# Performance work log

Hardware: AMD Instinct MI355X
Metric: run time of the kernel (lower is better)

The kernel has to match this reference:

```python
import jax, jax.numpy as jnp
import numpy as np

COMMITMENT_COST = 0.25


def setup_inputs() -> dict:
    key = jax.random.key(0)
    k1, k2 = jax.random.split(key)
    inputs = jax.random.normal(k1, (32, 1024, 256), dtype=jnp.float32)
    codebook = jax.random.normal(k2, (8192, 256), dtype=jnp.float32)
    return {"inputs": inputs, "codebook": codebook}


def reference(inputs, codebook):
    input_shape = inputs.shape
    D = codebook.shape[1]
    K = codebook.shape[0]
    flat = inputs.reshape(-1, D)                      # [N, D]
    N = flat.shape[0]

    distances = (
        jnp.sum(flat * flat, axis=1, keepdims=True)
        + jnp.sum(codebook * codebook, axis=1)
        - 2.0 * flat @ codebook.T
    )                                                  # [N, K]
    idx = jnp.argmin(distances, axis=1)               # [N]

    # gather (equivalent to one-hot @ codebook)
    quantized = jnp.take(codebook, idx, axis=0).reshape(input_shape)

    # straight-through estimator
    quantized_st = inputs + jax.lax.stop_gradient(quantized - inputs)

    e_latent_loss = jnp.mean((jax.lax.stop_gradient(quantized_st) - inputs) ** 2)
    q_latent_loss = jnp.mean((quantized - jax.lax.stop_gradient(inputs)) ** 2)
    commitment_loss = COMMITMENT_COST * e_latent_loss
    codebook_loss = q_latent_loss
    vq_loss = commitment_loss + codebook_loss

    # perplexity of codebook usage (avg one-hot probs)
    counts = jnp.zeros((K,), dtype=inputs.dtype).at[idx].add(1.0)
    avg_probs = counts / N
    perplexity = jnp.exp(-jnp.sum(avg_probs * jnp.log(avg_probs + 1e-10)))

    tokens = idx.reshape(input_shape[:-1])
    return quantized_st, tokens, vq_loss, commitment_loss, codebook_loss, perplexity
```

## Files before the change

### kernel.cpp

```cpp
#include <hip/hip_runtime.h>
#include <stdint.h>

typedef unsigned short u16;
typedef unsigned long long u64;

#define N_ROWS 32768
#define DIM 256
#define K_CODES 8192
#define TAU 0.3f

#define A_OFF     0ull
#define B_OFF     16777216ull
#define CN_OFF    20971520ull
#define PART1_OFF 21004288ull
#define PART2_OFF 22052864ull
#define IDX_OFF   22577152ull
#define HIST_OFF  22708224ull
#define CNT_OFF   22740992ull
#define FLAG_OFF  22741008ull
#define LOSS_OFF  22872080ull
#define CBT_OFF   23068672ull
#define GMIN2_OFF 31457280ull

#define OUT_Q 0
#define OUT_T 8388608
#define OUT_S 8421376

#define BM 128
#define BNT 64
#define JSPLIT 4
#define NJC ((K_CODES / JSPLIT) / BNT)
#define RSPLIT 4

#define PACK_INF ((((u64)0xFF800000u) << 32) | 0xFFFFFFFFull)

typedef _Float16 half8 __attribute__((ext_vector_type(8)));
typedef float floatx4 __attribute__((ext_vector_type(4)));

__device__ __forceinline__ void gload_lds16(const void* g, void* l) {
    __builtin_amdgcn_global_load_lds(
        (const __attribute__((address_space(1))) void*)g,
        (__attribute__((address_space(3))) void*)l,
        16, 0, 0);
}

__device__ __forceinline__ unsigned sortable(float v) {
    unsigned u = __float_as_uint(v);
    return (u & 0x80000000u) ? ~u : (u | 0x80000000u);
}
__device__ __forceinline__ float unsortable(unsigned u) {
    return (u & 0x80000000u) ? __uint_as_float(u & 0x7fffffffu) : __uint_as_float(~u);
}
__device__ __forceinline__ u64 shfl64x(u64 v, int m) {
    return ((u64)(unsigned)__shfl_xor((int)(v >> 32), m, 64) << 32) |
           (unsigned)__shfl_xor((int)(v & 0xffffffffu), m, 64);
}
__device__ __forceinline__ u64 u64min(u64 a, u64 b) { return a < b ? a : b; }
__device__ __forceinline__ u64 u64max(u64 a, u64 b) { return a > b ? a : b; }

__global__ void prep(const float* __restrict__ inp, const float* __restrict__ cb,
                     u16* __restrict__ A, u16* __restrict__ B, float* __restrict__ cn) {
    int g = blockIdx.x * 256 + threadIdx.x;
    int row = g >> 5;
    int kc = (g & 31) << 3;
    bool isA = row < N_ROWS;
    const float* src = isA ? inp + (size_t)row * DIM + kc
                           : cb + (size_t)(row - N_ROWS) * DIM + kc;
    u16* dst = isA ? A + (size_t)row * DIM + kc
                   : B + (size_t)(row - N_ROWS) * DIM + kc;
    float4 x0 = *(const float4*)(src);
    float4 x1 = *(const float4*)(src + 4);
    float xs[8] = {x0.x, x0.y, x0.z, x0.w, x1.x, x1.y, x1.z, x1.w};
    half8 hv;
    float s = 0.f;
#pragma unroll
    for (int i = 0; i < 8; ++i) {
        hv[i] = (_Float16)xs[i];
        s = fmaf(xs[i], xs[i], s);
    }
    *(half8*)(dst) = hv;
    if (!isA) {
#pragma unroll
        for (int m = 1; m <= 16; m <<= 1) s += __shfl_xor(s, m, 64);
        if ((g & 31) == 0) cn[row - N_ROWS] = s;
    }
}

__global__ void transpose_cb(const float* __restrict__ cb, float* __restrict__ cbT) {
    __shared__ float tile[64][65];
    const int tid = threadIdx.x;
    const int tj = blockIdx.x * 64;
    const int td = blockIdx.y * 64;
    const int c = (tid & 15) * 4;
    const int r0 = tid >> 4;
#pragma unroll
    for (int p = 0; p < 4; ++p) {
        int r = p * 16 + r0;
        float4 v = *(const float4*)(cb + (size_t)(tj + r) * DIM + td + c);
        tile[r][c] = v.x; tile[r][c + 1] = v.y; tile[r][c + 2] = v.z; tile[r][c + 3] = v.w;
    }
    __syncthreads();
#pragma unroll
    for (int p = 0; p < 4; ++p) {
        int rr = p * 16 + r0;
        float4 w = {tile[c][rr], tile[c + 1][rr], tile[c + 2][rr], tile[c + 3][rr]};
        *(float4*)(cbT + (size_t)(td + rr) * K_CODES + tj + c) = w;
    }
}

#define STAGE_B(BUFP, JCV)                                                    \
    {                                                                         \
        const u16* bsrc = B + (size_t)(jBase + (JCV) * BNT) * DIM;            \
        _Pragma("unroll")                                                     \
        for (int r_ = 0; r_ < 4; ++r_) {                                      \
            int idx_ = r_ * 512 + tid;                                        \
            int col_ = idx_ >> 5;                                             \
            int sc_ = idx_ & 31;                                              \
            int csrc_ = (sc_ & 24) | ((sc_ & 7) ^ (col_ & 7));                \
            gload_lds16(bsrc + (size_t)col_ * DIM + csrc_ * 8,                \
                        (char*)(BUFP) + idx_ * 16);                           \
        }                                                                     \
    }

#define TOP2(JT, CNV)                                                         \
    {                                                                         \
        unsigned jj = (unsigned)(jBase + (JT) * BNT + colLoc);                \
        _Pragma("unroll")                                                     \
        for (int mi_ = 0; mi_ < 4; ++mi_) {                                   \
            _Pragma("unroll")                                                 \
            for (int r_ = 0; r_ < 4; ++r_) {                                  \
                int tr_ = mi_ * 4 + r_;                                       \
                float val_ = fmaf(-2.0f, acc[mi_][r_], (CNV));                \
                float nd2_ = __builtin_amdgcn_fmed3f(d1[tr_], d2[tr_], val_); \
                bool lt_ = val_ < d1[tr_];                                    \
                d1[tr_] = fminf(d1[tr_], val_);                               \
                idxr[tr_] = lt_ ? jj : idxr[tr_];                             \
                d2[tr_] = nd2_;                                               \
            }                                                                 \
        }                                                                     \
    }

__launch_bounds__(512, 2)
__global__ void vq_pass1(const u16* __restrict__ A, const u16* __restrict__ B,
                         const float* __restrict__ cn,
                         u64* __restrict__ part1, float* __restrict__ part2) {
    __shared__ __align__(16) _Float16 lsB[2][BNT * DIM];

    const int tid = threadIdx.x;
    const int lane = tid & 63;
    const int w = tid >> 6;
    const int wm = w >> 2;
    const int wn = w & 3;
    const int l15 = lane & 15;
    const int quad = lane >> 4;
    const int xm = l15 & 7;
    const int colLoc = wn * 16 + l15;
    const int rowBase = blockIdx.x * BM;
    const int jBase = blockIdx.y * (K_CODES / JSPLIT);

    STAGE_B(lsB[0], 0);
    float cn_c = cn[jBase + colLoc];

    half8 af[4][8];
    {
        const u16* aRow = A + (size_t)(rowBase + wm * 64 + l15) * DIM + quad * 8;
#pragma unroll
        for (int mi = 0; mi < 4; ++mi)
#pragma unroll
            for (int ks = 0; ks < 8; ++ks)
                af[mi][ks] = *(const half8*)(aRow + (size_t)mi * 16 * DIM + ks * 32);
    }

    float d1[16], d2[16];
    unsigned idxr[16];
#pragma unroll
    for (int i = 0; i < 16; ++i) {
        d1[i] = __builtin_inff(); d2[i] = __builtin_inff(); idxr[i] = 0xffffffffu;
    }
    floatx4 acc[4];
    float cn_p = 0.f, cn_n = 0.f;

#pragma unroll 1
    for (int jc = 0; jc < NJC; ++jc) {
        if (jc < NJC - 1) {
            STAGE_B(lsB[(jc + 1) & 1], jc + 1);
            cn_n = cn[jBase + (jc + 1) * BNT + colLoc];
        }
        if (jc > 0) TOP2(jc - 1, cn_p);
        if (jc < NJC - 1) asm volatile("s_waitcnt vmcnt(5)" ::: "memory");
        else              asm volatile("s_waitcnt vmcnt(0)" ::: "memory");
        __builtin_amdgcn_s_barrier();

        const _Float16* bcur = lsB[jc & 1];
#pragma unroll
        for (int mi = 0; mi < 4; ++mi) acc[mi] = (floatx4){0.f, 0.f, 0.f, 0.f};
#pragma unroll
        for (int ks = 0; ks < 8; ++ks) {
            const int c = ks * 4 + quad;
            const int scw = (c & 24) | ((c & 7) ^ xm);
            half8 bfv = *(const half8*)((const char*)bcur + colLoc * 512 + scw * 16);
#pragma unroll
            for (int mi = 0; mi < 4; ++mi)
                acc[mi] = __builtin_amdgcn_mfma_f32_16x16x32_f16(
                    af[mi][ks], bfv, acc[mi], 0, 0, 0);
        }
        __builtin_amdgcn_s_barrier();
        cn_p = cn_c; cn_c = cn_n;
    }
    TOP2(NJC - 1, cn_p);

    u64 m1[16];
#pragma unroll
    for (int tr = 0; tr < 16; ++tr)
        m1[tr] = ((u64)sortable(d1[tr]) << 32) | idxr[tr];
#pragma unroll
    for (int m = 1; m <= 8; m <<= 1)
#pragma unroll
        for (int tr = 0; tr < 16; ++tr) {
            u64 o1 = shfl64x(m1[tr], m);
            float o2 = __shfl_xor(d2[tr], m, 64);
            u64 n1 = u64min(m1[tr], o1);
            float big = unsortable((unsigned)(u64max(m1[tr], o1) >> 32));
            d2[tr] = fminf(big, fminf(d2[tr], o2));
            m1[tr] = n1;
        }

    u64* t1 = (u64*)lsB[0];
    float* t2 = (float*)((char*)lsB[0] + 4 * BM * 8);
    __syncthreads();
    if (l15 == 0) {
#pragma unroll
        for (int tr = 0; tr < 16; ++tr) {
            int rl = wm * 64 + (tr >> 2) * 16 + quad * 4 + (tr & 3);
            t1[wn * BM + rl] = m1[tr];
            t2[wn * BM + rl] = d2[tr];
        }
    }
    __syncthreads();
    if (tid < BM) {
        u64 b1 = t1[tid];
        float b2 = t2[tid];
#pragma unroll
        for (int y = 1; y < 4; ++y) {
            u64 o1 = t1[y * BM + tid];
            float o2 = t2[y * BM + tid];
            u64 n1 = u64min(b1, o1);
            float big = unsortable((unsigned)(u64max(b1, o1) >> 32));
            b2 = fminf(big, fminf(b2, o2));
            b1 = n1;
        }
        size_t p = (size_t)(rowBase + tid) * JSPLIT + blockIdx.y;
        part1[p] = b1;
        part2[p] = b2;
    }
}

__global__ void vq_merge(const u64* __restrict__ part1, const float* __restrict__ part2,
                         unsigned* __restrict__ idx32,
                         int* __restrict__ flaglist, int* __restrict__ cnt) {
    int row = blockIdx.x * 256 + threadIdx.x;
    u64 m1 = PACK_INF;
    float f2 = __builtin_inff();
#pragma unroll
    for (int y = 0; y < JSPLIT; ++y) {
        u64 p1 = part1[(size_t)row * JSPLIT + y];
        float p2 = part2[(size_t)row * JSPLIT + y];
        u64 n1 = u64min(m1, p1);
        float big = unsortable((unsigned)(u64max(m1, p1) >> 32));
        f2 = fminf(big, fminf(f2, p2));
        m1 = n1;
    }
    idx32[row] = (unsigned)(m1 & 0xffffffffu);
    float f1 = unsortable((unsigned)(m1 >> 32));
    if (f2 - f1 < TAU) {
        int p = atomicAdd(cnt, 1);
        flaglist[p] = row;
    }
}

__global__ void vq_recompute(const float* __restrict__ inp, const float* __restrict__ cbT,
                             const float* __restrict__ cn, const int* __restrict__ flaglist,
                             const int* __restrict__ cnt, u64* __restrict__ gmin2) {
    __shared__ float xsT[DIM][8];
    __shared__ u64 wred[8][8];
    const int tid = threadIdx.x;
    const int w = tid >> 6, lane = tid & 63;
    const int n = *cnt;
    const int base = blockIdx.x * 8;
    if (base >= n) return;

    {
        int li = base + w;
        int row = flaglist[li < n ? li : (n - 1)];
        float4 a = ((const float4*)(inp + (size_t)row * DIM))[lane];
        int d0 = lane * 4;
        xsT[d0 + 0][w] = a.x; xsT[d0 + 1][w] = a.y;
        xsT[d0 + 2][w] = a.z; xsT[d0 + 3][w] = a.w;
    }
    __syncthreads();

    const int cbase = blockIdx.y * (K_CODES / RSPLIT) + tid * 4;
    float4 acc[8];
#pragma unroll
    for (int r = 0; r < 8; ++r) acc[r] = (float4){0.f, 0.f, 0.f, 0.f};

    float4 cv = *(const float4*)(cbT + cbase);
#pragma unroll 4
    for (int d = 0; d < DIM - 1; ++d) {
        float4 nx = *(const float4*)(cbT + (size_t)(d + 1) * K_CODES + cbase);
        float4 xa = *(const float4*)&xsT[d][0];
        float4 xb = *(const float4*)&xsT[d][4];
        float xv[8] = {xa.x, xa.y, xa.z, xa.w, xb.x, xb.y, xb.z, xb.w};
#pragma unroll
        for (int r = 0; r < 8; ++r) {
            acc[r].x = fmaf(xv[r], cv.x, acc[r].x);
            acc[r].y = fmaf(xv[r], cv.y, acc[r].y);
            acc[r].z = fmaf(xv[r], cv.z, acc[r].z);
            acc[r].w = fmaf(xv[r], cv.w, acc[r].w);
        }
        cv = nx;
    }
    {
        const int d = DIM - 1;
        float4 xa = *(const float4*)&xsT[d][0];
        float4 xb = *(const float4*)&xsT[d][4];
        float xv[8] = {xa.x, xa.y, xa.z, xa.w, xb.x, xb.y, xb.z, xb.w};
#pragma unroll
        for (int r = 0; r < 8; ++r) {
            acc[r].x = fmaf(xv[r], cv.x, acc[r].x);
            acc[r].y = fmaf(xv[r], cv.y, acc[r].y);
            acc[r].z = fmaf(xv[r], cv.z, acc[r].z);
            acc[r].w = fmaf(xv[r], cv.w, acc[r].w);
        }
    }

    u64 best[8];
    float4 cn4 = *(const float4*)(cn + cbase);
#pragma unroll
    for (int r = 0; r < 8; ++r) {
        float d0 = cn4.x - 2.0f * acc[r].x;
        float d1 = cn4.y - 2.0f * acc[r].y;
        float d2 = cn4.z - 2.0f * acc[r].z;
        float d3 = cn4.w - 2.0f * acc[r].w;
        u64 b = ((u64)sortable(d0) << 32) | (unsigned)(cbase + 0);
        b = u64min(b, ((u64)sortable(d1) << 32) | (unsigned)(cbase + 1));
        b = u64min(b, ((u64)sortable(d2) << 32) | (unsigned)(cbase + 2));
        b = u64min(b, ((u64)sortable(d3) << 32) | (unsigned)(cbase + 3));
        best[r] = b;
    }

#pragma unroll
    for (int m = 1; m <= 32; m <<= 1)
#pragma unroll
        for (int r = 0; r < 8; ++r) best[r] = u64min(best[r], shfl64x(best[r], m));
    if (lane < 8) wred[w][lane] = best[lane];
    __syncthreads();
    if (tid < 8 && base + tid < n) {
        u64 b = wred[0][tid];
#pragma unroll
        for (int ww = 1; ww < 8; ++ww) b = u64min(b, wred[ww][tid]);
        atomicMin(&gmin2[flaglist[base + tid]], b);
    }
}

__global__ void vq_writeback(const u64* __restrict__ gmin2, const int* __restrict__ flaglist,
                             const int* __restrict__ cnt, unsigned* __restrict__ idx32) {
    int i = blockIdx.x * 256 + threadIdx.x;
    if (i < *cnt) {
        int row = flaglist[i];
        idx32[row] = (unsigned)(gmin2[row] & 0xffffffffull);
    }
}

__global__ void vq_gather(const float* __restrict__ inp, const float* __restrict__ cb,
                          const unsigned* __restrict__ idx32, float* __restrict__ out,
                          float* __restrict__ losspart, unsigned int* __restrict__ hist) {
    __shared__ float red[4];
    int w = threadIdx.x >> 6, lane = threadIdx.x & 63;
    int i = blockIdx.x * 4 + w;
    unsigned idx = idx32[i];
    float4 c = ((const float4*)(cb + (size_t)idx * DIM))[lane];
    float4 x = ((const float4*)(inp + (size_t)i * DIM))[lane];
    ((float4*)(out + OUT_Q))[(size_t)i * 64 + lane] = c;
    float dx = c.x - x.x, dy = c.y - x.y, dz = c.z - x.z, dw = c.w - x.w;
    float s = dx * dx + dy * dy + dz * dz + dw * dw;
#pragma unroll
    for (int m = 32; m; m >>= 1) s += __shfl_xor(s, m, 64);
    if (lane == 0) {
        out[OUT_T + i] = (float)idx;
        red[w] = s;
        atomicAdd(&hist[idx], 1u);
    }
    __syncthreads();
    if (threadIdx.x == 0)
        losspart[blockIdx.x] = red[0] + red[1] + red[2] + red[3];
}

__global__ void vq_finalize(const unsigned int* __restrict__ hist,
                            const float* __restrict__ losspart, float* __restrict__ out) {
    __shared__ float redp[256], redl[256];
    int tid = threadIdx.x;
    float sp = 0.f, sl = 0.f;
    for (int k = tid; k < K_CODES; k += 256) {
        float p = (float)hist[k] * (1.0f / (float)N_ROWS);
        sp += p * logf(p + 1e-10f);
        sl += losspart[k];
    }
    redp[tid] = sp; redl[tid] = sl;
    __syncthreads();
    for (int st = 128; st; st >>= 1) {
        if (tid < st) { redp[tid] += redp[tid + st]; redl[tid] += redl[tid + st]; }
        __syncthreads();
    }
    if (tid == 0) {
        float perp = expf(-redp[0]);
        float e = redl[0] / 8388608.0f;
        out[OUT_S + 0] = 1.25f * e;
        out[OUT_S + 1] = 0.25f * e;
        out[OUT_S + 2] = e;
        out[OUT_S + 3] = perp;
    }
}

extern "C" void kernel_launch(void* const* d_in, const int* in_sizes, int n_in,
                              void* d_out, int out_size, void* d_ws, size_t ws_size,
                              hipStream_t stream) {
    const float* inp = (const float*)d_in[0];
    const float* cb = (const float*)d_in[1];
    float* out = (float*)d_out;
    char* ws = (char*)d_ws;
    u16* A = (u16*)(ws + A_OFF);
    u16* B = (u16*)(ws + B_OFF);
    float* cn = (float*)(ws + CN_OFF);
    u64* part1 = (u64*)(ws + PART1_OFF);
    float* part2 = (float*)(ws + PART2_OFF);
    unsigned* idx32 = (unsigned*)(ws + IDX_OFF);
    unsigned int* hist = (unsigned int*)(ws + HIST_OFF);
    int* cnt = (int*)(ws + CNT_OFF);
    int* flaglist = (int*)(ws + FLAG_OFF);
    float* losspart = (float*)(ws + LOSS_OFF);
    float* cbT = (float*)(ws + CBT_OFF);
    u64* gmin2 = (u64*)(ws + GMIN2_OFF);

    hipMemsetAsync(hist, 0, K_CODES * 4 + 16, stream);
    hipMemsetAsync(gmin2, 0xFF, N_ROWS * 8, stream);

    prep<<<5120, 256, 0, stream>>>(inp, cb, A, B, cn);
    transpose_cb<<<dim3(K_CODES / 64, DIM / 64), 256, 0, stream>>>(cb, cbT);
    vq_pass1<<<dim3(N_ROWS / BM, JSPLIT), 512, 0, stream>>>(A, B, cn, part1, part2);
    vq_merge<<<N_ROWS / 256, 256, 0, stream>>>(part1, part2, idx32, flaglist, cnt);
    vq_recompute<<<dim3(N_ROWS / 8, RSPLIT), 512, 0, stream>>>(inp, cbT, cn, flaglist, cnt, gmin2);
    vq_writeback<<<N_ROWS / 256, 256, 0, stream>>>(gmin2, flaglist, cnt, idx32);
    vq_gather<<<N_ROWS / 4, 256, 0, stream>>>(inp, cb, idx32, out, losspart, hist);
    vq_finalize<<<1, 256, 0, stream>>>(hist, losspart, out);
}
```

Baseline: 410.8 us.

## Drop LDS staging of codebook tiles; load B fragments directly from global

The main distance GEMM kernel no longer double-buffers codebook tiles into shared memory with async global-to-LDS loads and barriers. Each wave now reads its B fragments straight from global memory (relying on L2/L1 caching), with 64-row blocks of 256 threads instead of 128-row blocks of 512. This removes barrier and LDS traffic and the software pipelining, but gives up overlap of loads with MFMA, and halving rows per block doubles the codebook reads from global/L2.

```diff
diff --git a/kernel.cpp b/kernel.cpp
--- a/kernel.cpp
+++ b/kernel.cpp
@@ -26,23 +26,15 @@
 #define OUT_T 8388608
 #define OUT_S 8421376
 
-#define BM 128
-#define BNT 64
+#define BMR 64
 #define JSPLIT 4
-#define NJC ((K_CODES / JSPLIT) / BNT)
+#define NJC ((K_CODES / JSPLIT) / 64)
 #define RSPLIT 4
 
 #define PACK_INF ((((u64)0xFF800000u) << 32) | 0xFFFFFFFFull)
 
 typedef _Float16 half8 __attribute__((ext_vector_type(8)));
 typedef float floatx4 __attribute__((ext_vector_type(4)));
-
-__device__ __forceinline__ void gload_lds16(const void* g, void* l) {
-    __builtin_amdgcn_global_load_lds(
-        (const __attribute__((address_space(1))) void*)g,
-        (__attribute__((address_space(3))) void*)l,
-        16, 0, 0);
-}
 
 __device__ __forceinline__ unsigned sortable(float v) {
     unsigned u = __float_as_uint(v);
@@ -108,67 +100,30 @@
     }
 }
 
-#define STAGE_B(BUFP, JCV)                                                    \
-    {                                                                         \
-        const u16* bsrc = B + (size_t)(jBase + (JCV) * BNT) * DIM;            \
-        _Pragma("unroll")                                                     \
-        for (int r_ = 0; r_ < 4; ++r_) {                                      \
-            int idx_ = r_ * 512 + tid;                                        \
-            int col_ = idx_ >> 5;                                             \
-            int sc_ = idx_ & 31;                                              \
-            int csrc_ = (sc_ & 24) | ((sc_ & 7) ^ (col_ & 7));                \
-            gload_lds16(bsrc + (size_t)col_ * DIM + csrc_ * 8,                \
-                        (char*)(BUFP) + idx_ * 16);                           \
-        }                                                                     \
-    }
-
-#define TOP2(JT, CNV)                                                         \
-    {                                                                         \
-        unsigned jj = (unsigned)(jBase + (JT) * BNT + colLoc);                \
-        _Pragma("unroll")                                                     \
-        for (int mi_ = 0; mi_ < 4; ++mi_) {                                   \
-            _Pragma("unroll")                                                 \
-            for (int r_ = 0; r_ < 4; ++r_) {                                  \
-                int tr_ = mi_ * 4 + r_;                                       \
-                float val_ = fmaf(-2.0f, acc[mi_][r_], (CNV));                \
-                float nd2_ = __builtin_amdgcn_fmed3f(d1[tr_], d2[tr_], val_); \
-                bool lt_ = val_ < d1[tr_];                                    \
-                d1[tr_] = fminf(d1[tr_], val_);                               \
-                idxr[tr_] = lt_ ? jj : idxr[tr_];                             \
-                d2[tr_] = nd2_;                                               \
-            }                                                                 \
-        }                                                                     \
-    }
-
-__launch_bounds__(512, 2)
+__launch_bounds__(256, 4)
 __global__ void vq_pass1(const u16* __restrict__ A, const u16* __restrict__ B,
                          const float* __restrict__ cn,
                          u64* __restrict__ part1, float* __restrict__ part2) {
-    __shared__ __align__(16) _Float16 lsB[2][BNT * DIM];
+    __shared__ u64 t1[4][64];
+    __shared__ float t2[4][64];
 
     const int tid = threadIdx.x;
     const int lane = tid & 63;
     const int w = tid >> 6;
-    const int wm = w >> 2;
-    const int wn = w & 3;
     const int l15 = lane & 15;
     const int quad = lane >> 4;
-    const int xm = l15 & 7;
-    const int colLoc = wn * 16 + l15;
-    const int rowBase = blockIdx.x * BM;
+    const int colLoc = w * 16 + l15;
+    const int rowBase = blockIdx.x * BMR;
     const int jBase = blockIdx.y * (K_CODES / JSPLIT);
-
-    STAGE_B(lsB[0], 0);
-    float cn_c = cn[jBase + colLoc];
 
     half8 af[4][8];
     {
-        const u16* aRow = A + (size_t)(rowBase + wm * 64 + l15) * DIM + quad * 8;
+        const u16* aRow = A + (size_t)(rowBase + l15) * DIM + quad * 8;
 #pragma unroll
         for (int mi = 0; mi < 4; ++mi)
 #pragma unroll
             for (int ks = 0; ks < 8; ++ks)
-                af[mi][ks] = *(const half8*)(aRow + (size_t)mi * 16 * DIM + ks * 32);
+                af[mi][ks] = *(const half8*)(aRow + mi * 16 * DIM + ks * 32);
     }
 
     float d1[16], d2[16];
@@ -177,37 +132,42 @@
     for (int i = 0; i < 16; ++i) {
         d1[i] = __builtin_inff(); d2[i] = __builtin_inff(); idxr[i] = 0xffffffffu;
     }
-    floatx4 acc[4];
-    float cn_p = 0.f, cn_n = 0.f;
+
+    const u16* bLane = B + (size_t)(jBase + colLoc) * DIM + quad * 8;
+    const float* cnLane = cn + jBase + colLoc;
 
 #pragma unroll 1
     for (int jc = 0; jc < NJC; ++jc) {
-        if (jc < NJC - 1) {
-            STAGE_B(lsB[(jc + 1) & 1], jc + 1);
-            cn_n = cn[jBase + (jc + 1) * BNT + colLoc];
-        }
-        if (jc > 0) TOP2(jc - 1, cn_p);
-        if (jc < NJC - 1) asm volatile("s_waitcnt vmcnt(5)" ::: "memory");
-        else              asm volatile("s_waitcnt vmcnt(0)" ::: "memory");
-        __builtin_amdgcn_s_barrier();
-
-        const _Float16* bcur = lsB[jc & 1];
+        const u16* bT = bLane + (size_t)jc * 64 * DIM;
+        float cnj = cnLane[jc * 64];
+
+        floatx4 acc[4];
 #pragma unroll
         for (int mi = 0; mi < 4; ++mi) acc[mi] = (floatx4){0.f, 0.f, 0.f, 0.f};
 #pragma unroll
         for (int ks = 0; ks < 8; ++ks) {
-            const int c = ks * 4 + quad;
-            const int scw = (c & 24) | ((c & 7) ^ xm);
-            half8 bfv = *(const half8*)((const char*)bcur + colLoc * 512 + scw * 16);
+            half8 bf = *(const half8*)(bT + ks * 32);
 #pragma unroll
             for (int mi = 0; mi < 4; ++mi)
                 acc[mi] = __builtin_amdgcn_mfma_f32_16x16x32_f16(
-                    af[mi][ks], bfv, acc[mi], 0, 0, 0);
-        }
-        __builtin_amdgcn_s_barrier();
-        cn_p = cn_c; cn_c = cn_n;
-    }
-    TOP2(NJC - 1, cn_p);
+                    af[mi][ks], bf, acc[mi], 0, 0, 0);
+        }
+
+        unsigned jj = (unsigned)(jBase + jc * 64 + colLoc);
+#pragma unroll
+        for (int mi = 0; mi < 4; ++mi) {
+#pragma unroll
+            for (int r = 0; r < 4; ++r) {
+                int tr = mi * 4 + r;
+                float val = fmaf(-2.0f, acc[mi][r], cnj);
+                float nd2 = __builtin_amdgcn_fmed3f(d1[tr], d2[tr], val);
+                bool lt = val < d1[tr];
+                d1[tr] = fminf(d1[tr], val);
+                idxr[tr] = lt ? jj : idxr[tr];
+                d2[tr] = nd2;
+            }
+        }
+    }
 
     u64 m1[16];
 #pragma unroll
@@ -225,25 +185,22 @@
             m1[tr] = n1;
         }
 
-    u64* t1 = (u64*)lsB[0];
-    float* t2 = (float*)((char*)lsB[0] + 4 * BM * 8);
-    __syncthreads();
     if (l15 == 0) {
 #pragma unroll
         for (int tr = 0; tr < 16; ++tr) {
-            int rl = wm * 64 + (tr >> 2) * 16 + quad * 4 + (tr & 3);
-            t1[wn * BM + rl] = m1[tr];
-            t2[wn * BM + rl] = d2[tr];
-        }
-    }
-    __syncthreads();
-    if (tid < BM) {
-        u64 b1 = t1[tid];
-        float b2 = t2[tid];
+            int rl = (tr >> 2) * 16 + quad * 4 + (tr & 3);
+            t1[w][rl] = m1[tr];
+            t2[w][rl] = d2[tr];
+        }
+    }
+    __syncthreads();
+    if (tid < BMR) {
+        u64 b1 = t1[0][tid];
+        float b2 = t2[0][tid];
 #pragma unroll
         for (int y = 1; y < 4; ++y) {
-            u64 o1 = t1[y * BM + tid];
-            float o2 = t2[y * BM + tid];
+            u64 o1 = t1[y][tid];
+            float o2 = t2[y][tid];
             u64 n1 = u64min(b1, o1);
             float big = unsortable((unsigned)(u64max(b1, o1) >> 32));
             b2 = fminf(big, fminf(b2, o2));
@@ -447,7 +404,7 @@
 
     prep<<<5120, 256, 0, stream>>>(inp, cb, A, B, cn);
     transpose_cb<<<dim3(K_CODES / 64, DIM / 64), 256, 0, stream>>>(cb, cbT);
-    vq_pass1<<<dim3(N_ROWS / BM, JSPLIT), 512, 0, stream>>>(A, B, cn, part1, part2);
+    vq_pass1<<<dim3(N_ROWS / BMR, JSPLIT), 256, 0, stream>>>(A, B, cn, part1, part2);
     vq_merge<<<N_ROWS / 256, 256, 0, stream>>>(part1, part2, idx32, flaglist, cnt);
     vq_recompute<<<dim3(N_ROWS / 8, RSPLIT), 512, 0, stream>>>(inp, cbT, cn, flaglist, cnt, gmin2);
     vq_writeback<<<N_ROWS / 256, 256, 0, stream>>>(gmin2, flaglist, cnt, idx32);
```

Measured after the change: 1.107 ms. 169% more time.

## Triple-buffer codebook tiles and overlap top-2 epilogue with next MFMA tile

Applied to the files above, without the earlier changes.

Moves the distance GEMM main loop from double to triple buffering of codebook tiles in LDS, prefetching two tiles ahead. It ping-pongs two accumulator sets so the top-2 reduction of the previous tile runs alongside the next tile's MFMAs, with one barrier per tile instead of two. Codebook norms are loaded into an LDS ring via async global-to-LDS loads, and MFMA sections get raised wave priority. This uses more LDS (48KB+ of B tiles per block) and more accumulator registers, which may pressure the 2-blocks-per-CU occupancy target.

```diff
diff --git a/kernel.cpp b/kernel.cpp
--- a/kernel.cpp
+++ b/kernel.cpp
@@ -42,6 +42,12 @@
         (const __attribute__((address_space(1))) void*)g,
         (__attribute__((address_space(3))) void*)l,
         16, 0, 0);
+}
+__device__ __forceinline__ void gload_lds4(const void* g, void* l) {
+    __builtin_amdgcn_global_load_lds(
+        (const __attribute__((address_space(1))) void*)g,
+        (__attribute__((address_space(3))) void*)l,
+        4, 0, 0);
 }
 
 __device__ __forceinline__ unsigned sortable(float v) {
@@ -110,41 +116,81 @@
 
 #define STAGE_B(BUFP, JCV)                                                    \
     {                                                                         \
-        const u16* bsrc = B + (size_t)(jBase + (JCV) * BNT) * DIM;            \
+        const u16* bsrc_ = B + (size_t)(jBase + (JCV) * BNT) * DIM;           \
         _Pragma("unroll")                                                     \
         for (int r_ = 0; r_ < 4; ++r_) {                                      \
             int idx_ = r_ * 512 + tid;                                        \
             int col_ = idx_ >> 5;                                             \
             int sc_ = idx_ & 31;                                              \
             int csrc_ = (sc_ & 24) | ((sc_ & 7) ^ (col_ & 7));                \
-            gload_lds16(bsrc + (size_t)col_ * DIM + csrc_ * 8,                \
+            gload_lds16(bsrc_ + (size_t)col_ * DIM + csrc_ * 8,               \
                         (char*)(BUFP) + idx_ * 16);                           \
         }                                                                     \
-    }
-
-#define TOP2(JT, CNV)                                                         \
+        gload_lds4(cn + jBase + (JCV) * BNT + lane,                           \
+                   &cnRing[(JCV) & 3][lane]);                                 \
+    }
+
+#define TOP2(JT, ACC, CNV)                                                    \
     {                                                                         \
-        unsigned jj = (unsigned)(jBase + (JT) * BNT + colLoc);                \
+        unsigned jj_ = (unsigned)(jBase + (JT) * BNT + colLoc);               \
         _Pragma("unroll")                                                     \
         for (int mi_ = 0; mi_ < 4; ++mi_) {                                   \
             _Pragma("unroll")                                                 \
             for (int r_ = 0; r_ < 4; ++r_) {                                  \
                 int tr_ = mi_ * 4 + r_;                                       \
-                float val_ = fmaf(-2.0f, acc[mi_][r_], (CNV));                \
+                float val_ = fmaf(-2.0f, ACC[mi_][r_], (CNV));                \
                 float nd2_ = __builtin_amdgcn_fmed3f(d1[tr_], d2[tr_], val_); \
                 bool lt_ = val_ < d1[tr_];                                    \
                 d1[tr_] = fminf(d1[tr_], val_);                               \
-                idxr[tr_] = lt_ ? jj : idxr[tr_];                             \
+                idxr[tr_] = lt_ ? jj_ : idxr[tr_];                            \
                 d2[tr_] = nd2_;                                               \
             }                                                                 \
         }                                                                     \
+    }
+
+#define MFMA_TILE(BP, ACC_C)                                                  \
+    {                                                                         \
+        _Pragma("unroll")                                                     \
+        for (int mi_ = 0; mi_ < 4; ++mi_)                                     \
+            ACC_C[mi_] = (floatx4){0.f, 0.f, 0.f, 0.f};                       \
+        __builtin_amdgcn_s_setprio(1);                                        \
+        _Pragma("unroll")                                                     \
+        for (int ks_ = 0; ks_ < 8; ++ks_) {                                   \
+            const int c_ = ks_ * 4 + quad;                                    \
+            const int scw_ = (c_ & 24) | ((c_ & 7) ^ xm);                     \
+            half8 bfv_ = *(const half8*)((const char*)(BP) + colLoc * 512 +   \
+                                         scw_ * 16);                          \
+            _Pragma("unroll")                                                 \
+            for (int mi_ = 0; mi_ < 4; ++mi_)                                 \
+                ACC_C[mi_] = __builtin_amdgcn_mfma_f32_16x16x32_f16(          \
+                    af[mi_][ks_], bfv_, ACC_C[mi_], 0, 0, 0);                 \
+        }                                                                     \
+        __builtin_amdgcn_s_setprio(0);                                        \
+    }
+
+#define TILE(JCV, ACC_C, ACC_P, DO_STAGE, DO_TOP2, WAITN)                     \
+    {                                                                         \
+        if (DO_STAGE) STAGE_B(bp2, (JCV) + 2);                                \
+        if (DO_TOP2) {                                                        \
+            float cnv_ = cnRing[((JCV) - 1) & 3][colLoc];                     \
+            TOP2((JCV) - 1, ACC_P, cnv_);                                     \
+        }                                                                     \
+        MFMA_TILE(bp0, ACC_C);                                                \
+        if ((WAITN) == 5) asm volatile("s_waitcnt vmcnt(5)" ::: "memory");    \
+        else if ((WAITN) == 0) asm volatile("s_waitcnt vmcnt(0)" ::: "memory");\
+        __builtin_amdgcn_s_barrier();                                         \
+        asm volatile("" ::: "memory");                                        \
+        { _Float16* tp_ = bp0; bp0 = bp1; bp1 = bp2; bp2 = tp_; }             \
     }
 
 __launch_bounds__(512, 2)
 __global__ void vq_pass1(const u16* __restrict__ A, const u16* __restrict__ B,
                          const float* __restrict__ cn,
                          u64* __restrict__ part1, float* __restrict__ part2) {
-    __shared__ __align__(16) _Float16 lsB[2][BNT * DIM];
+    __shared__ __align__(16) _Float16 lsB[3][BNT * DIM];
+    __shared__ float cnRing[4][BNT];
+    __shared__ u64 t1[8][64];
+    __shared__ float t2[8][64];
 
     const int tid = threadIdx.x;
     const int lane = tid & 63;
@@ -158,8 +204,9 @@
     const int rowBase = blockIdx.x * BM;
     const int jBase = blockIdx.y * (K_CODES / JSPLIT);
 
-    STAGE_B(lsB[0], 0);
-    float cn_c = cn[jBase + colLoc];
+    _Float16* bp0 = lsB[0];
+    _Float16* bp1 = lsB[1];
+    _Float16* bp2 = lsB[2];
 
     half8 af[4][8];
     {
@@ -177,37 +224,25 @@
     for (int i = 0; i < 16; ++i) {
         d1[i] = __builtin_inff(); d2[i] = __builtin_inff(); idxr[i] = 0xffffffffu;
     }
-    floatx4 acc[4];
-    float cn_p = 0.f, cn_n = 0.f;
+    floatx4 accA[4], accB[4];
+
+    STAGE_B(bp0, 0);
+    STAGE_B(bp1, 1);
+    asm volatile("s_waitcnt vmcnt(5)" ::: "memory");
+    __builtin_amdgcn_s_barrier();
+    asm volatile("" ::: "memory");
 
 #pragma unroll 1
-    for (int jc = 0; jc < NJC; ++jc) {
-        if (jc < NJC - 1) {
-            STAGE_B(lsB[(jc + 1) & 1], jc + 1);
-            cn_n = cn[jBase + (jc + 1) * BNT + colLoc];
-        }
-        if (jc > 0) TOP2(jc - 1, cn_p);
-        if (jc < NJC - 1) asm volatile("s_waitcnt vmcnt(5)" ::: "memory");
-        else              asm volatile("s_waitcnt vmcnt(0)" ::: "memory");
-        __builtin_amdgcn_s_barrier();
-
-        const _Float16* bcur = lsB[jc & 1];
-#pragma unroll
-        for (int mi = 0; mi < 4; ++mi) acc[mi] = (floatx4){0.f, 0.f, 0.f, 0.f};
-#pragma unroll
-        for (int ks = 0; ks < 8; ++ks) {
-            const int c = ks * 4 + quad;
-            const int scw = (c & 24) | ((c & 7) ^ xm);
-            half8 bfv = *(const half8*)((const char*)bcur + colLoc * 512 + scw * 16);
-#pragma unroll
-            for (int mi = 0; mi < 4; ++mi)
-                acc[mi] = __builtin_amdgcn_mfma_f32_16x16x32_f16(
-                    af[mi][ks], bfv, acc[mi], 0, 0, 0);
-        }
-        __builtin_amdgcn_s_barrier();
-        cn_p = cn_c; cn_c = cn_n;
-    }
-    TOP2(NJC - 1, cn_p);
+    for (int jc2 = 0; jc2 < NJC - 2; jc2 += 2) {
+        TILE(jc2,     accA, accB, true, (jc2 > 0), 5);
+        TILE(jc2 + 1, accB, accA, true, true,      5);
+    }
+    TILE(NJC - 2, accA, accB, false, true, 0);
+    TILE(NJC - 1, accB, accA, false, true, -1);
+    {
+        float cnv_ = cnRing[(NJC - 1) & 3][colLoc];
+        TOP2(NJC - 1, accB, cnv_);
+    }
 
     u64 m1[16];
 #pragma unroll
@@ -225,25 +260,24 @@
             m1[tr] = n1;
         }
 
-    u64* t1 = (u64*)lsB[0];
-    float* t2 = (float*)((char*)lsB[0] + 4 * BM * 8);
-    __syncthreads();
     if (l15 == 0) {
 #pragma unroll
         for (int tr = 0; tr < 16; ++tr) {
-            int rl = wm * 64 + (tr >> 2) * 16 + quad * 4 + (tr & 3);
-            t1[wn * BM + rl] = m1[tr];
-            t2[wn * BM + rl] = d2[tr];
+            int rl = (tr >> 2) * 16 + quad * 4 + (tr & 3);
+            t1[w][rl] = m1[tr];
+            t2[w][rl] = d2[tr];
         }
     }
     __syncthreads();
     if (tid < BM) {
-        u64 b1 = t1[tid];
-        float b2 = t2[tid];
+        int rg = tid >> 6;
+        int rl = tid & 63;
+        u64 b1 = t1[rg * 4][rl];
+        float b2 = t2[rg * 4][rl];
 #pragma unroll
         for (int y = 1; y < 4; ++y) {
-            u64 o1 = t1[y * BM + tid];
-            float o2 = t2[y * BM + tid];
+            u64 o1 = t1[rg * 4 + y][rl];
+            float o2 = t2[rg * 4 + y][rl];
             u64 n1 = u64min(b1, o1);
             float big = unsortable((unsigned)(u64max(b1, o1) >> 32));
             b2 = fminf(big, fminf(b2, o2));
```

Result: no change. 418.7 us (+1.9%).
